# Kernel tuning notes

Hardware: AMD Instinct MI355X
Metric: run time of the kernel (lower is better)

The kernel has to match this reference:

```python
import jax, jax.numpy as jnp
import numpy as np

B, N, E = 2, 2048, 2048
H, G, D = 16, 4, 128          # num_heads, num_kv_groups, head_dim = E // H
HID = 4 * E                    # GeGLU hidden width
EPS = 1e-6


def setup_inputs() -> dict:
    key = jax.random.key(0)
    ks = jax.random.split(key, 8)
    g = lambda k, shape: jax.random.normal(k, shape, jnp.float32) * 0.02
    return {
        "x": jax.random.normal(ks[0], (B, N, E), jnp.float32),
        "wq": g(ks[1], (E, H * D)),
        "wk": g(ks[2], (E, G * D)),
        "wv": g(ks[3], (E, G * D)),
        "wo": g(ks[4], (H * D, E)),
        "w1": g(ks[5], (E, 2 * HID)),   # GeGLU in-proj (value | gate)
        "w2": g(ks[6], (HID, E)),       # GeGLU out-proj
        "norm1_w": jnp.ones((E,), jnp.float32),
        "norm2_w": jnp.ones((E,), jnp.float32),
    }


def _rope_cos_sin(n, d, dtype):
    inv_freq = 1.0 / (10000.0 ** (jnp.arange(0, d, 2, dtype=jnp.float32) / d))
    freqs = jnp.arange(n, dtype=jnp.float32)[:, None] * inv_freq[None, :]  # [n, d/2]
    emb = jnp.concatenate([freqs, freqs], axis=-1)                          # [n, d]
    return jnp.cos(emb).astype(dtype), jnp.sin(emb).astype(dtype)


def _rotate_half(t):
    d2 = t.shape[-1] // 2
    return jnp.concatenate([-t[..., d2:], t[..., :d2]], axis=-1)


def _apply_rope(t, cos, sin):
    # t: [b, h, n, d]; cos/sin: [n, d]
    return t * cos + _rotate_half(t) * sin


def _rmsnorm(x, w):
    var = jnp.mean(jnp.square(x), axis=-1, keepdims=True)
    return x * jax.lax.rsqrt(var + EPS) * w


def reference(x, wq, wk, wv, wo, w1, w2, norm1_w, norm2_w):
    b, n, _ = x.shape
    # q = k = v = x reshaped into heads (pre-projection, as in source)
    qkv = x.reshape(b, n, H, D).transpose(0, 2, 1, 3)  # [b, H, n, D]
    cos, sin = _rope_cos_sin(n, D, x.dtype)
    q_r = _apply_rope(qkv, cos, sin)
    k_r = _apply_rope(qkv, cos, sin)
    # flatten back to [b, n, E]
    q_flat = q_r.transpose(0, 2, 1, 3).reshape(b, n, E)
    k_flat = k_r.transpose(0, 2, 1, 3).reshape(b, n, E)
    v_flat = x  # v untouched by RoPE; flatten == x

    # Grouped-query attention with internal projections
    qh = (q_flat @ wq).reshape(b, n, H, D).transpose(0, 2, 1, 3)       # [b, H, n, D]
    kh = (k_flat @ wk).reshape(b, n, G, D)                              # [b, n, G, D]
    vh = (v_flat @ wv).reshape(b, n, G, D)
    kh = jnp.repeat(kh, H // G, axis=2).transpose(0, 2, 1, 3)           # [b, H, n, D]
    vh = jnp.repeat(vh, H // G, axis=2).transpose(0, 2, 1, 3)

    scale = 1.0 / np.sqrt(D)
    scores = jnp.einsum('bhqd,bhkd->bhqk', qh, kh) * scale
    attn = jax.nn.softmax(scores, axis=-1)                               # [b, H, n, n]
    ctx = jnp.einsum('bhqk,bhkd->bhqd', attn, vh)
    attn_out = ctx.transpose(0, 2, 1, 3).reshape(b, n, H * D) @ wo      # [b, n, E]

    x1 = _rmsnorm(x + attn_out, norm1_w)

    # GeGLU FFN
    uv = x1 @ w1
    u, gate = jnp.split(uv, 2, axis=-1)
    fc = (u * jax.nn.gelu(gate)) @ w2

    x2 = _rmsnorm(x1 + fc, norm2_w)
    return (x2, (k_flat, v_flat), attn)
```

## Files before the change

kernel.cpp:

```cpp
#include <hip/hip_runtime.h>
#include <hip/hip_bf16.h>


using f32x4  = __attribute__((ext_vector_type(4))) float;
using bf16x8 = __attribute__((ext_vector_type(8))) short;
using bf16x4 = __attribute__((ext_vector_type(4))) short;
using u16x4  = __attribute__((ext_vector_type(4))) unsigned short;

#define DEV __device__ __forceinline__

#define ASYNC16(lds, g)                                                        \
  __builtin_amdgcn_global_load_lds(                                           \
      (const __attribute__((address_space(1))) void*)(g),                      \
      (__attribute__((address_space(3))) void*)(lds), 16, 0, 0)

DEV unsigned short f2bf(float f) {
  unsigned int u = __float_as_uint(f);
  return (unsigned short)((u + 0x7fffu + ((u >> 16) & 1u)) >> 16);
}
DEV float bf2f(unsigned short h) {
  return __uint_as_float(((unsigned int)h) << 16);
}

DEV float waveRedSum(float v) {
#pragma unroll
  for (int o = 32; o; o >>= 1) v += __shfl_xor(v, o);
  return v;
}

__global__ __launch_bounds__(256) void kconvAll(
    const float* __restrict__ wq, const float* __restrict__ wk,
    const float* __restrict__ wv, const float* __restrict__ wo,
    const float* __restrict__ w1, unsigned short* __restrict__ dst) {
  __shared__ float tile[32][33];
  int bx = blockIdx.x * 32;
  int by = blockIdx.y * 32;
  const float* src; int nsrc, c0;
  if (bx < 2048)      { src = wq; nsrc = 2048;  c0 = bx; }
  else if (bx < 2560) { src = wk; nsrc = 512;   c0 = bx - 2048; }
  else if (bx < 3072) { src = wv; nsrc = 512;   c0 = bx - 2560; }
  else if (bx < 5120) { src = wo; nsrc = 2048;  c0 = bx - 3072; }
  else                { src = w1; nsrc = 16384; c0 = bx - 5120; }
  int tx = threadIdx.x & 31;
  int ty = threadIdx.x >> 5;
#pragma unroll
  for (int i = 0; i < 32; i += 8)
    tile[ty + i][tx] = src[(size_t)(by + ty + i) * nsrc + c0 + tx];
  __syncthreads();
#pragma unroll
  for (int i = 0; i < 32; i += 8)
    dst[(size_t)(bx + ty + i) * 2048 + by + tx] = f2bf(tile[tx][ty + i]);
}

__global__ __launch_bounds__(256) void kconvT(const float* __restrict__ in,
                                              unsigned short* __restrict__ out,
                                              int K, int N) {
  __shared__ float tile[32][33];
  int bx = blockIdx.x * 32;
  int by = blockIdx.y * 32;
  int tx = threadIdx.x & 31;
  int ty = threadIdx.x >> 5;
#pragma unroll
  for (int i = 0; i < 32; i += 8)
    tile[ty + i][tx] = in[(size_t)(by + ty + i) * N + bx + tx];
  __syncthreads();
#pragma unroll
  for (int i = 0; i < 32; i += 8)
    out[(size_t)(bx + ty + i) * K + by + tx] = f2bf(tile[tx][ty + i]);
}

__global__ __launch_bounds__(256) void krope(const float* __restrict__ x,
                                             float* __restrict__ kout,
                                             float* __restrict__ vout,
                                             unsigned short* __restrict__ xq,
                                             unsigned short* __restrict__ xb) {
  int idx = blockIdx.x * 256 + threadIdx.x;
  int f  = idx & 63;
  int h  = (idx >> 6) & 15;
  int bn = idx >> 10;
  int n  = bn & 2047;
  size_t base = (size_t)bn * 2048 + h * 128;
  float inv = exp2f((float)f * (-13.287712379549449f / 64.0f));
  float ang = (float)n * inv;
  float c = cosf(ang), s = sinf(ang);
  float a = x[base + f], b = x[base + f + 64];
  float k1 = a * c - b * s;
  float k2 = b * c + a * s;
  __builtin_nontemporal_store(k1, kout + base + f);
  __builtin_nontemporal_store(k2, kout + base + f + 64);
  xq[base + f]      = f2bf(k1);
  xq[base + f + 64] = f2bf(k2);
  __builtin_nontemporal_store(a, vout + base + f);
  __builtin_nontemporal_store(b, vout + base + f + 64);
  xb[base + f]      = f2bf(a);
  xb[base + f + 64] = f2bf(b);
}

__global__ __launch_bounds__(256) void krms1(const float* __restrict__ x,
                                             const float* __restrict__ ao,
                                             const float* __restrict__ w,
                                             unsigned short* __restrict__ x1b) {
  size_t row = blockIdx.x;
  const f32x4* xp = (const f32x4*)(x + row * 2048);
  const f32x4* ap = (const f32x4*)(ao + row * 2048);
  int tid = threadIdx.x;
  f32x4 t0 = xp[tid * 2] + ap[tid * 2];
  f32x4 t1 = xp[tid * 2 + 1] + ap[tid * 2 + 1];
  float ss = 0.f;
#pragma unroll
  for (int i = 0; i < 4; ++i) ss += t0[i] * t0[i] + t1[i] * t1[i];
  ss = waveRedSum(ss);
  __shared__ float red[4];
  int wid = tid >> 6, lane = tid & 63;
  if (!lane) red[wid] = ss;
  __syncthreads();
  ss = red[0] + red[1] + red[2] + red[3];
  float rr = rsqrtf(ss * (1.0f / 2048.0f) + 1e-6f);
  const f32x4* wp = (const f32x4*)w;
  f32x4 w0 = wp[tid * 2], w1 = wp[tid * 2 + 1];
  u16x4 o0, o1;
#pragma unroll
  for (int i = 0; i < 4; ++i) {
    o0[i] = f2bf(t0[i] * rr * w0[i]);
    o1[i] = f2bf(t1[i] * rr * w1[i]);
  }
  u16x4* op = (u16x4*)(x1b + row * 2048);
  op[tid * 2] = o0;
  op[tid * 2 + 1] = o1;
}

__global__ __launch_bounds__(256) void krms2(const unsigned short* __restrict__ x1b,
                                             const unsigned short* __restrict__ fc,
                                             const float* __restrict__ w,
                                             float* __restrict__ out) {
  size_t row = blockIdx.x;
  const u16x4* xp = (const u16x4*)(x1b + row * 2048);
  const u16x4* fp = (const u16x4*)(fc + row * 2048);
  int tid = threadIdx.x;
  u16x4 a0 = xp[tid * 2], a1 = xp[tid * 2 + 1];
  u16x4 b0 = fp[tid * 2], b1 = fp[tid * 2 + 1];
  f32x4 t0, t1;
#pragma unroll
  for (int i = 0; i < 4; ++i) {
    t0[i] = bf2f(a0[i]) + bf2f(b0[i]);
    t1[i] = bf2f(a1[i]) + bf2f(b1[i]);
  }
  float ss = 0.f;
#pragma unroll
  for (int i = 0; i < 4; ++i) ss += t0[i] * t0[i] + t1[i] * t1[i];
  ss = waveRedSum(ss);
  __shared__ float red[4];
  int wid = tid >> 6, lane = tid & 63;
  if (!lane) red[wid] = ss;
  __syncthreads();
  ss = red[0] + red[1] + red[2] + red[3];
  float rr = rsqrtf(ss * (1.0f / 2048.0f) + 1e-6f);
  const f32x4* wp = (const f32x4*)w;
  f32x4 w0 = wp[tid * 2], w1 = wp[tid * 2 + 1];
  f32x4* op = (f32x4*)(out + row * 2048);
  f32x4 o0 = t0 * rr * w0;
  f32x4 o1 = t1 * rr * w1;
  __builtin_nontemporal_store(o0, op + tid * 2);
  __builtin_nontemporal_store(o1, op + tid * 2 + 1);
}

__global__ __launch_bounds__(256, 2) void kvproj(
    const unsigned short* __restrict__ xq, const unsigned short* __restrict__ xb,
    const unsigned short* __restrict__ wkT, const unsigned short* __restrict__ wvT,
    unsigned short* __restrict__ kh, unsigned short* __restrict__ vhT) {
  const bool isV = blockIdx.z != 0;
  const unsigned short* A  = isV ? xb : xq;
  const unsigned short* Bt = isV ? wvT : wkT;
  __shared__ unsigned short As[128 * 32];
  __shared__ unsigned short Bs[128 * 32];
  const int tid = threadIdx.x;
  const int bm0 = blockIdx.y * 128, bn0 = blockIdx.x * 128;

  f32x4 acc[4][4] = {};

  const int lane = tid & 63, wid = tid >> 6;
  const int wr = wid >> 1, wc = wid & 1;
  const int lr = lane & 15, kq = lane >> 4;
  const int srow = tid >> 2;
  const int scol = (tid & 3) * 8;
  unsigned short* AsW = As + tid * 8;
  unsigned short* BsW = Bs + tid * 8;

  for (int kt = 0; kt < 2048; kt += 32) {
    ASYNC16(AsW,        A + (size_t)(bm0 + srow)      * 2048 + kt + scol);
    ASYNC16(AsW + 2048, A + (size_t)(bm0 + srow + 64) * 2048 + kt + scol);
    ASYNC16(BsW,        Bt + (size_t)(bn0 + srow)      * 2048 + kt + scol);
    ASYNC16(BsW + 2048, Bt + (size_t)(bn0 + srow + 64) * 2048 + kt + scol);
    __syncthreads();
    bf16x8 afr[4], bfr[4];
#pragma unroll
    for (int i = 0; i < 4; ++i)
      afr[i] = *(const bf16x8*)&As[(wr * 64 + i * 16 + lr) * 32 + kq * 8];
#pragma unroll
    for (int j = 0; j < 4; ++j)
      bfr[j] = *(const bf16x8*)&Bs[(wc * 64 + j * 16 + lr) * 32 + kq * 8];
#pragma unroll
    for (int i = 0; i < 4; ++i)
#pragma unroll
      for (int j = 0; j < 4; ++j)
        acc[i][j] = __builtin_amdgcn_mfma_f32_16x16x32_bf16(afr[i], bfr[j],
                                                            acc[i][j], 0, 0, 0);
    __syncthreads();
  }

#pragma unroll
  for (int i = 0; i < 4; ++i)
#pragma unroll
    for (int j = 0; j < 4; ++j) {
      int rowb = bm0 + wr * 64 + i * 16 + kq * 4;
      int col = bn0 + wc * 64 + j * 16 + lr;
#pragma unroll
      for (int r = 0; r < 4; ++r) {
        unsigned short v = f2bf(acc[i][j][r]);
        if (isV) vhT[(size_t)col * 4096 + (rowb + r)] = v;
        else     kh[(size_t)(rowb + r) * 512 + col] = v;
      }
    }
}

__global__ __launch_bounds__(512, 4) void kattn(
    const unsigned short* __restrict__ qh,
    const unsigned short* __restrict__ kh,
    const unsigned short* __restrict__ vT,
    float* __restrict__ attn,
    unsigned short* __restrict__ ctx) {
  __shared__ __align__(16) char U[65536];
  __shared__ __align__(16) char Vb[16384];
  float* redm = (float*)Vb;
  float* reds = redm + 128;

  const int tid = threadIdx.x;
  const int lane = tid & 63, w = tid >> 6;
  const int lr = lane & 15, kq = lane >> 4;
  const int bid = blockIdx.x;
  const int g8 = bid & 7;
  const int j  = bid >> 3;
  const int bz = g8 >> 2;
  const int gz = g8 & 3;
  const int hz = gz * 4 + (j & 3);
  const int q0 = (j >> 2) << 4;
  const int z  = bz * 16 + hz;

  const unsigned short* Aq =
      qh + ((size_t)(bz * 2048 + q0 + lr) * 2048 + hz * 128);
  bf16x8 qfr[4];
#pragma unroll
  for (int kk = 0; kk < 4; ++kk)
    qfr[kk] = *(const bf16x8*)(Aq + kk * 32 + kq * 8);

  const unsigned short* Kb =
      kh + ((size_t)(bz * 2048) * 512 + gz * 128);
  int krow[4], kcs[4];
#pragma unroll
  for (int R = 0; R < 4; ++R) {
    int idx = R * 64 + lane;
    krow[R] = idx >> 4;
    kcs[R] = (idx & 15) ^ (krow[R] & 7);
  }
  auto stageK = [&](int buf, int t) {
#pragma unroll
    for (int R = 0; R < 4; ++R)
      ASYNC16(U + buf * 32768 + w * 4096 + (R * 64 + lane) * 16,
              Kb + (size_t)(t * 128 + w * 16 + krow[R]) * 512 + kcs[R] * 8);
  };

  f32x4 acc[16];
#pragma unroll
  for (int t = 0; t < 16; ++t) acc[t] = f32x4{0.f, 0.f, 0.f, 0.f};

  stageK(0, 0);
  stageK(1, 1);
#pragma unroll
  for (int t = 0; t < 16; ++t) {
    if (t < 15) asm volatile("s_waitcnt vmcnt(4)" ::: "memory");
    else        asm volatile("s_waitcnt vmcnt(0)" ::: "memory");
    __builtin_amdgcn_sched_barrier(0);
    const char* Kw = U + (t & 1) * 32768 + w * 4096;
    bf16x8 kfr[4];
#pragma unroll
    for (int kk = 0; kk < 4; ++kk) {
      int cch = (kk * 4 + kq) ^ (lr & 7);
      kfr[kk] = *(const bf16x8*)(Kw + lr * 256 + cch * 16);
    }
    asm volatile("s_waitcnt lgkmcnt(0)" ::: "memory");
    __builtin_amdgcn_sched_barrier(0);
    if (t + 2 < 16) stageK(t & 1, t + 2);
    __builtin_amdgcn_s_setprio(1);
#pragma unroll
    for (int kk = 0; kk < 4; ++kk)
      acc[t] = __builtin_amdgcn_mfma_f32_16x16x32_bf16(kfr[kk], qfr[kk],
                                                       acc[t], 0, 0, 0);
    __builtin_amdgcn_s_setprio(0);
  }

  const float scale = 0.08838834764831845f;
  float mx = -3.4e38f;
#pragma unroll
  for (int t = 0; t < 16; ++t) {
    acc[t] *= scale;
#pragma unroll
    for (int r = 0; r < 4; ++r) mx = fmaxf(mx, acc[t][r]);
  }
  mx = fmaxf(mx, __shfl_xor(mx, 16));
  mx = fmaxf(mx, __shfl_xor(mx, 32));
  if (kq == 0) redm[w * 16 + lr] = mx;
  __syncthreads();
  mx = redm[lr];
#pragma unroll
  for (int ww = 1; ww < 8; ++ww) mx = fmaxf(mx, redm[ww * 16 + lr]);

  float sm = 0.f;
#pragma unroll
  for (int t = 0; t < 16; ++t) {
#pragma unroll
    for (int r = 0; r < 4; ++r) {
      float e = __expf(acc[t][r] - mx);
      acc[t][r] = e;
      sm += e;
    }
  }
  sm += __shfl_xor(sm, 16);
  sm += __shfl_xor(sm, 32);
  if (kq == 0) reds[w * 16 + lr] = sm;
  __syncthreads();
  float smt = reds[lr];
#pragma unroll
  for (int ww = 1; ww < 8; ++ww) smt += reds[ww * 16 + lr];
  float inv = 1.0f / smt;

  float* arow = attn + (((size_t)z * 2048 + q0 + lr) * 2048);
#pragma unroll
  for (int t = 0; t < 16; ++t) {
    int key = t * 128 + w * 16 + kq * 4;
    f32x4 p = acc[t] * inv;
    __builtin_nontemporal_store(p, (f32x4*)(arow + key));
    bf16x4 pb;
#pragma unroll
    for (int r = 0; r < 4; ++r) pb[r] = (short)f2bf(p[r]);
    int c8 = key >> 3;
    *(bf16x4*)(U + lr * 4096 + ((c8 ^ (lr & 7)) << 4) + ((key & 7) << 1)) = pb;
  }
  __syncthreads();

  const unsigned short* Bv = vT + (size_t)gz * 524288 + bz * 2048;
  const int d0 = w * 16;
  const int vd = lane >> 2;
  const int vcs = (lane & 3) ^ (vd & 3);
  auto stageV = [&](int buf, int t) {
    ASYNC16(Vb + buf * 8192 + w * 1024 + lane * 16,
            Bv + (size_t)(d0 + vd) * 4096 + t * 32 + vcs * 8);
  };

  f32x4 cfr = {};
  stageV(0, 0);
  stageV(1, 1);
#pragma unroll
  for (int t = 0; t < 64; ++t) {
    if (t < 63) asm volatile("s_waitcnt vmcnt(1)" ::: "memory");
    else        asm volatile("s_waitcnt vmcnt(0)" ::: "memory");
    __builtin_amdgcn_sched_barrier(0);
    int c8 = t * 4 + kq;
    bf16x8 pfr = *(const bf16x8*)(U + lr * 4096 + ((c8 ^ (lr & 7)) << 4));
    const char* Vw = Vb + (t & 1) * 8192 + w * 1024;
    bf16x8 vfr = *(const bf16x8*)(Vw + lr * 64 + ((kq ^ (lr & 3)) << 4));
    asm volatile("s_waitcnt lgkmcnt(0)" ::: "memory");
    __builtin_amdgcn_sched_barrier(0);
    if (t + 2 < 64) stageV(t & 1, t + 2);
    __builtin_amdgcn_s_setprio(1);
    cfr = __builtin_amdgcn_mfma_f32_16x16x32_bf16(pfr, vfr, cfr, 0, 0, 0);
    __builtin_amdgcn_s_setprio(0);
  }
#pragma unroll
  for (int r = 0; r < 4; ++r) {
    int q = kq * 4 + r;
    ctx[((size_t)(bz * 2048 + q0 + q) * 2048) + hz * 128 + d0 + lr] =
        f2bf(cfr[r]);
  }
}

template <bool OUT_BF16>
__global__ __launch_bounds__(512, 2) void gemm128(
    const unsigned short* __restrict__ A, const unsigned short* __restrict__ Bt,
    void* __restrict__ C_, int K, int lda, int ldb, int ldc) {
  __shared__ unsigned short As[2][128 * 64];
  __shared__ unsigned short Bs[2][128 * 64];
  const int tid = threadIdx.x;
  const int bid = blockIdx.x;
  const int xcd = bid & 7, ii = bid >> 3;
  const int my = (xcd >> 1) * 8 + (ii & 7);
  const int nx = (xcd & 1) * 8 + (ii >> 3);
  const int bm0 = my * 128, bn0 = nx * 128;
  const int lane = tid & 63, wid = tid >> 6;
  const int wr = wid >> 2, wc = wid & 3;
  const int lr = lane & 15, kq = lane >> 4;

  f32x4 acc[4][2] = {};

  int sArow[2], sAcc[2];
#pragma unroll
  for (int R = 0; R < 2; ++R) {
    int c = R * 512 + tid;
    sArow[R] = c >> 3;
    sAcc[R]  = (c & 7) ^ (sArow[R] & 7);
  }

  auto stage = [&](int buf, int k0) {
#pragma unroll
    for (int R = 0; R < 2; ++R)
      ASYNC16(&As[buf][(R * 512 + tid) * 8],
              A + (size_t)(bm0 + sArow[R]) * lda + k0 + sAcc[R] * 8);
#pragma unroll
    for (int R = 0; R < 2; ++R)
      ASYNC16(&Bs[buf][(R * 512 + tid) * 8],
              Bt + (size_t)(bn0 + sArow[R]) * ldb + k0 + sAcc[R] * 8);
  };

  const int NT = K >> 6;
  stage(0, 0);
  stage(1, 64);
  int cur = 0;
  for (int t = 0; t < NT; ++t) {
    if (t + 1 < NT) asm volatile("s_waitcnt vmcnt(4)" ::: "memory");
    else            asm volatile("s_waitcnt vmcnt(0)" ::: "memory");
    __builtin_amdgcn_sched_barrier(0);
    __builtin_amdgcn_s_barrier();
    __builtin_amdgcn_sched_barrier(0);
    const unsigned short* Ac = As[cur];
    const unsigned short* Bc = Bs[cur];
    bf16x8 afr0[4], bfr0[2];
#pragma unroll
    for (int i = 0; i < 4; ++i) {
      int row = wr * 64 + i * 16 + lr;
      afr0[i] = *(const bf16x8*)&Ac[(row * 8 + (kq ^ (row & 7))) * 8];
    }
#pragma unroll
    for (int j2 = 0; j2 < 2; ++j2) {
      int brow = wc * 32 + j2 * 16 + lr;
      bfr0[j2] = *(const bf16x8*)&Bc[(brow * 8 + (kq ^ (brow & 7))) * 8];
    }
    __builtin_amdgcn_s_setprio(1);
#pragma unroll
    for (int j2 = 0; j2 < 2; ++j2)
#pragma unroll
      for (int i = 0; i < 4; ++i)
        acc[i][j2] = __builtin_amdgcn_mfma_f32_16x16x32_bf16(afr0[i], bfr0[j2],
                                                             acc[i][j2], 0, 0, 0);
    __builtin_amdgcn_s_setprio(0);
    bf16x8 afr1[4], bfr1[2];
#pragma unroll
    for (int i = 0; i < 4; ++i) {
      int row = wr * 64 + i * 16 + lr;
      afr1[i] = *(const bf16x8*)&Ac[(row * 8 + ((4 + kq) ^ (row & 7))) * 8];
    }
#pragma unroll
    for (int j2 = 0; j2 < 2; ++j2) {
      int brow = wc * 32 + j2 * 16 + lr;
      bfr1[j2] = *(const bf16x8*)&Bc[(brow * 8 + ((4 + kq) ^ (brow & 7))) * 8];
    }
    asm volatile("s_waitcnt lgkmcnt(0)" ::: "memory");
    __builtin_amdgcn_sched_barrier(0);
    __builtin_amdgcn_s_barrier();
    __builtin_amdgcn_sched_barrier(0);
    if (t + 2 < NT) stage(cur, (t + 2) << 6);
    __builtin_amdgcn_s_setprio(1);
#pragma unroll
    for (int j2 = 0; j2 < 2; ++j2)
#pragma unroll
      for (int i = 0; i < 4; ++i)
        acc[i][j2] = __builtin_amdgcn_mfma_f32_16x16x32_bf16(afr1[i], bfr1[j2],
                                                             acc[i][j2], 0, 0, 0);
    __builtin_amdgcn_s_setprio(0);
    cur ^= 1;
  }

#pragma unroll
  for (int i = 0; i < 4; ++i)
#pragma unroll
    for (int j = 0; j < 2; ++j) {
      int rowb = bm0 + wr * 64 + i * 16 + kq * 4;
      int col = bn0 + wc * 32 + j * 16 + lr;
#pragma unroll
      for (int r = 0; r < 4; ++r) {
        if constexpr (OUT_BF16)
          ((unsigned short*)C_)[(size_t)(rowb + r) * ldc + col] = f2bf(acc[i][j][r]);
        else
          ((float*)C_)[(size_t)(rowb + r) * ldc + col] = acc[i][j][r];
      }
    }
}

__global__ __launch_bounds__(512, 2) void gemm_geglu256(
    const unsigned short* __restrict__ A, const unsigned short* __restrict__ B1,
    const unsigned short* __restrict__ B2, unsigned short* __restrict__ H_,
    int K, int lda, int ldb, int ldc) {
  __shared__ unsigned short As[2][256 * 64];
  __shared__ unsigned short B1s[2][128 * 64];
  __shared__ unsigned short B2s[2][128 * 64];
  const int tid = threadIdx.x;
  const int bid = blockIdx.x;
  const int xcd = bid & 7, ii = bid >> 3;
  const int my = (xcd >> 2) * 8 + (ii & 7);
  const int nx = (xcd & 3) * 16 + (ii >> 3);
  const int bm0 = my * 256, bn0 = nx * 128;
  const int lane = tid & 63, wid = tid >> 6;
  const int wr = wid >> 2, wc = wid & 3;
  const int lr = lane & 15, kq = lane >> 4;

  f32x4 accu[8][2] = {};
  f32x4 accg[8][2] = {};

  int sArow[4], sAcc[4], sBrow[2], sBcc[2];
#pragma unroll
  for (int R = 0; R < 4; ++R) {
    int c = R * 512 + tid;
    sArow[R] = c >> 3;
    sAcc[R]  = (c & 7) ^ (sArow[R] & 7);
  }
#pragma unroll
  for (int R = 0; R < 2; ++R) {
    int c = R * 512 + tid;
    sBrow[R] = c >> 3;
    sBcc[R]  = (c & 7) ^ (sBrow[R] & 7);
  }

  auto stage = [&](int buf, int k0) {
#pragma unroll
    for (int R = 0; R < 4; ++R)
      ASYNC16(&As[buf][(R * 512 + tid) * 8],
              A + (size_t)(bm0 + sArow[R]) * lda + k0 + sAcc[R] * 8);
#pragma unroll
    for (int R = 0; R < 2; ++R)
      ASYNC16(&B1s[buf][(R * 512 + tid) * 8],
              B1 + (size_t)(bn0 + sBrow[R]) * ldb + k0 + sBcc[R] * 8);
#pragma unroll
    for (int R = 0; R < 2; ++R)
      ASYNC16(&B2s[buf][(R * 512 + tid) * 8],
              B2 + (size_t)(bn0 + sBrow[R]) * ldb + k0 + sBcc[R] * 8);
  };

  const int NT = K >> 6;
  stage(0, 0);
  stage(1, 64);
  int cur = 0;
  for (int t = 0; t < NT; ++t) {
    if (t + 1 < NT) asm volatile("s_waitcnt vmcnt(8)" ::: "memory");
    else            asm volatile("s_waitcnt vmcnt(0)" ::: "memory");
    __builtin_amdgcn_sched_barrier(0);
    __builtin_amdgcn_s_barrier();
    __builtin_amdgcn_sched_barrier(0);
    const unsigned short* Ac = As[cur];
    const unsigned short* B1c = B1s[cur];
    const unsigned short* B2c = B2s[cur];
    bf16x8 afr0[8], b10[2], b20[2];
#pragma unroll
    for (int i = 0; i < 8; ++i) {
      int row = wr * 128 + i * 16 + lr;
      afr0[i] = *(const bf16x8*)&Ac[(row * 8 + (kq ^ (row & 7))) * 8];
    }
#pragma unroll
    for (int j2 = 0; j2 < 2; ++j2) {
      int brow = wc * 32 + j2 * 16 + lr;
      b10[j2] = *(const bf16x8*)&B1c[(brow * 8 + (kq ^ (brow & 7))) * 8];
      b20[j2] = *(const bf16x8*)&B2c[(brow * 8 + (kq ^ (brow & 7))) * 8];
    }
    __builtin_amdgcn_s_setprio(1);
#pragma unroll
    for (int j2 = 0; j2 < 2; ++j2)
#pragma unroll
      for (int i = 0; i < 8; ++i) {
        accu[i][j2] = __builtin_amdgcn_mfma_f32_16x16x32_bf16(afr0[i], b10[j2],
                                                              accu[i][j2], 0, 0, 0);
        accg[i][j2] = __builtin_amdgcn_mfma_f32_16x16x32_bf16(afr0[i], b20[j2],
                                                              accg[i][j2], 0, 0, 0);
      }
    __builtin_amdgcn_s_setprio(0);
    bf16x8 afr1[8], b11[2], b21[2];
#pragma unroll
    for (int i = 0; i < 8; ++i) {
      int row = wr * 128 + i * 16 + lr;
      afr1[i] = *(const bf16x8*)&Ac[(row * 8 + ((4 + kq) ^ (row & 7))) * 8];
    }
#pragma unroll
    for (int j2 = 0; j2 < 2; ++j2) {
      int brow = wc * 32 + j2 * 16 + lr;
      b11[j2] = *(const bf16x8*)&B1c[(brow * 8 + ((4 + kq) ^ (brow & 7))) * 8];
      b21[j2] = *(const bf16x8*)&B2c[(brow * 8 + ((4 + kq) ^ (brow & 7))) * 8];
    }
    asm volatile("s_waitcnt lgkmcnt(0)" ::: "memory");
    __builtin_amdgcn_sched_barrier(0);
    __builtin_amdgcn_s_barrier();
    __builtin_amdgcn_sched_barrier(0);
    if (t + 2 < NT) stage(cur, (t + 2) << 6);
    __builtin_amdgcn_s_setprio(1);
#pragma unroll
    for (int j2 = 0; j2 < 2; ++j2)
#pragma unroll
      for (int i = 0; i < 8; ++i) {
        accu[i][j2] = __builtin_amdgcn_mfma_f32_16x16x32_bf16(afr1[i], b11[j2],
                                                              accu[i][j2], 0, 0, 0);
        accg[i][j2] = __builtin_amdgcn_mfma_f32_16x16x32_bf16(afr1[i], b21[j2],
                                                              accg[i][j2], 0, 0, 0);
      }
    __builtin_amdgcn_s_setprio(0);
    cur ^= 1;
  }

#pragma unroll
  for (int i = 0; i < 8; ++i)
#pragma unroll
    for (int j = 0; j < 2; ++j) {
      int rowb = bm0 + wr * 128 + i * 16 + kq * 4;
      int col = bn0 + wc * 32 + j * 16 + lr;
#pragma unroll
      for (int r = 0; r < 4; ++r) {
        float u = accu[i][j][r];
        float g = accg[i][j][r];
        float tv = tanhf(0.7978845608028654f * (g + 0.044715f * g * g * g));
        float hv = u * 0.5f * g * (1.0f + tv);
        H_[(size_t)(rowb + r) * ldc + col] = f2bf(hv);
      }
    }
}

extern "C" void kernel_launch(void* const* d_in, const int* in_sizes, int n_in,
                              void* d_out, int out_size, void* d_ws, size_t ws_size,
                              hipStream_t stream) {
  const float* x   = (const float*)d_in[0];
  const float* wq  = (const float*)d_in[1];
  const float* wk  = (const float*)d_in[2];
  const float* wv  = (const float*)d_in[3];
  const float* wo  = (const float*)d_in[4];
  const float* w1  = (const float*)d_in[5];
  const float* w2  = (const float*)d_in[6];
  const float* n1w = (const float*)d_in[7];
  const float* n2w = (const float*)d_in[8];

  float* out    = (float*)d_out;
  float* x2_out = out;
  float* k_out  = out + 8388608;
  float* v_out  = out + 16777216;
  float* attn   = out + 25165824;

  char* ws = (char*)d_ws;
  unsigned short* wqT  = (unsigned short*)(ws + 0);
  unsigned short* wkT  = (unsigned short*)(ws + 8388608);
  unsigned short* wvT  = (unsigned short*)(ws + 10485760);
  unsigned short* woT  = (unsigned short*)(ws + 12582912);
  unsigned short* w1T  = (unsigned short*)(ws + 20971520);
  unsigned short* w2T  = (unsigned short*)(ws + 88080384);
  unsigned short* qh   = (unsigned short*)(ws + 121634816);
  unsigned short* kh   = (unsigned short*)(ws + 138412032);
  unsigned short* vhT  = (unsigned short*)(ws + 142606336);
  unsigned short* ctx  = (unsigned short*)(ws + 146800640);
  float*          ao   = (float*)(ws + 163577856);
  unsigned short* hbuf = (unsigned short*)(ws + 121634816);
  unsigned short* x1b  = (unsigned short*)(ws + 197132288);
  unsigned short* fc   = (unsigned short*)(ws + 213909504);

  unsigned short* xb = (unsigned short*)attn;
  unsigned short* xq = xb + 8388608;

  dim3 blk(256);
  dim3 blk512(512);

  kconvAll<<<dim3(672, 64), blk, 0, stream>>>(wq, wk, wv, wo, w1, wqT);
  kconvT<<<dim3(64, 256), blk, 0, stream>>>(w2, w2T, 8192, 2048);

  krope<<<16384, blk, 0, stream>>>(x, k_out, v_out, xq, xb);

  gemm128<true><<<dim3(512), blk512, 0, stream>>>(
      xq, wqT, qh, 2048, 2048, 2048, 2048);
  kvproj<<<dim3(4, 32, 2), blk, 0, stream>>>(xq, xb, wkT, wvT, kh, vhT);

  kattn<<<dim3(4096), blk512, 0, stream>>>(qh, kh, vhT, attn, ctx);

  gemm128<false><<<dim3(512), blk512, 0, stream>>>(
      ctx, woT, (void*)ao, 2048, 2048, 2048, 2048);
  krms1<<<4096, blk, 0, stream>>>(x, ao, n1w, x1b);
  gemm_geglu256<<<dim3(1024), blk512, 0, stream>>>(
      x1b, w1T, w1T + 16777216, hbuf, 2048, 2048, 2048, 8192);
  gemm128<true><<<dim3(512), blk512, 0, stream>>>(
      hbuf, w2T, fc, 8192, 8192, 8192, 2048);
  krms2<<<4096, blk, 0, stream>>>(x1b, fc, n2w, x2_out);
}
```

Before: 913.2 us.

## Double-buffer kvproj loads, merge softmax reductions, emit bf16 attention-out projection

The K/V projection GEMM now double-buffers its LDS tiles, using a swizzled layout and explicit vmcnt waits so global-to-LDS copies overlap with MFMA work. The attention kernel merges its max and sum cross-wave reductions into one barrier by rescaling per-wave partial sums with an online-softmax correction. The Wo projection now writes bf16 instead of fp32, which halves the traffic into the RMSNorm kernel at the cost of rounding the attention output before the residual add.

```diff
diff --git a/kernel.cpp b/kernel.cpp
--- a/kernel.cpp
+++ b/kernel.cpp
@@ -97,15 +97,21 @@
 }
 
 __global__ __launch_bounds__(256) void krms1(const float* __restrict__ x,
-                                             const float* __restrict__ ao,
+                                             const unsigned short* __restrict__ ao,
                                              const float* __restrict__ w,
                                              unsigned short* __restrict__ x1b) {
   size_t row = blockIdx.x;
   const f32x4* xp = (const f32x4*)(x + row * 2048);
-  const f32x4* ap = (const f32x4*)(ao + row * 2048);
+  const u16x4* ap = (const u16x4*)(ao + row * 2048);
   int tid = threadIdx.x;
-  f32x4 t0 = xp[tid * 2] + ap[tid * 2];
-  f32x4 t1 = xp[tid * 2 + 1] + ap[tid * 2 + 1];
+  f32x4 x0 = xp[tid * 2], x1v = xp[tid * 2 + 1];
+  u16x4 a0 = ap[tid * 2], a1 = ap[tid * 2 + 1];
+  f32x4 t0, t1;
+#pragma unroll
+  for (int i = 0; i < 4; ++i) {
+    t0[i] = x0[i] + bf2f(a0[i]);
+    t1[i] = x1v[i] + bf2f(a1[i]);
+  }
   float ss = 0.f;
 #pragma unroll
   for (int i = 0; i < 4; ++i) ss += t0[i] * t0[i] + t1[i] * t1[i];
@@ -171,8 +177,8 @@
   const bool isV = blockIdx.z != 0;
   const unsigned short* A  = isV ? xb : xq;
   const unsigned short* Bt = isV ? wvT : wkT;
-  __shared__ unsigned short As[128 * 32];
-  __shared__ unsigned short Bs[128 * 32];
+  __shared__ unsigned short As[2][128 * 32];
+  __shared__ unsigned short Bs[2][128 * 32];
   const int tid = threadIdx.x;
   const int bm0 = blockIdx.y * 128, bn0 = blockIdx.x * 128;
 
@@ -181,31 +187,62 @@
   const int lane = tid & 63, wid = tid >> 6;
   const int wr = wid >> 1, wc = wid & 1;
   const int lr = lane & 15, kq = lane >> 4;
-  const int srow = tid >> 2;
-  const int scol = (tid & 3) * 8;
-  unsigned short* AsW = As + tid * 8;
-  unsigned short* BsW = Bs + tid * 8;
-
-  for (int kt = 0; kt < 2048; kt += 32) {
-    ASYNC16(AsW,        A + (size_t)(bm0 + srow)      * 2048 + kt + scol);
-    ASYNC16(AsW + 2048, A + (size_t)(bm0 + srow + 64) * 2048 + kt + scol);
-    ASYNC16(BsW,        Bt + (size_t)(bn0 + srow)      * 2048 + kt + scol);
-    ASYNC16(BsW + 2048, Bt + (size_t)(bn0 + srow + 64) * 2048 + kt + scol);
-    __syncthreads();
+
+  int srow[2], scc[2];
+#pragma unroll
+  for (int R = 0; R < 2; ++R) {
+    int slot = R * 256 + tid;
+    srow[R] = slot >> 2;
+    scc[R]  = (slot & 3) ^ (srow[R] & 3);
+  }
+  auto stage = [&](int buf, int k0) {
+#pragma unroll
+    for (int R = 0; R < 2; ++R)
+      ASYNC16(&As[buf][(R * 256 + tid) * 8],
+              A + (size_t)(bm0 + srow[R]) * 2048 + k0 + scc[R] * 8);
+#pragma unroll
+    for (int R = 0; R < 2; ++R)
+      ASYNC16(&Bs[buf][(R * 256 + tid) * 8],
+              Bt + (size_t)(bn0 + srow[R]) * 2048 + k0 + scc[R] * 8);
+  };
+
+  const int NT = 64;
+  stage(0, 0);
+  stage(1, 32);
+  int cur = 0;
+  for (int t = 0; t < NT; ++t) {
+    if (t + 1 < NT) asm volatile("s_waitcnt vmcnt(4)" ::: "memory");
+    else            asm volatile("s_waitcnt vmcnt(0)" ::: "memory");
+    __builtin_amdgcn_sched_barrier(0);
+    __builtin_amdgcn_s_barrier();
+    __builtin_amdgcn_sched_barrier(0);
+    const unsigned short* Ac = As[cur];
+    const unsigned short* Bc = Bs[cur];
     bf16x8 afr[4], bfr[4];
 #pragma unroll
-    for (int i = 0; i < 4; ++i)
-      afr[i] = *(const bf16x8*)&As[(wr * 64 + i * 16 + lr) * 32 + kq * 8];
-#pragma unroll
-    for (int j = 0; j < 4; ++j)
-      bfr[j] = *(const bf16x8*)&Bs[(wc * 64 + j * 16 + lr) * 32 + kq * 8];
+    for (int i = 0; i < 4; ++i) {
+      int row = wr * 64 + i * 16 + lr;
+      afr[i] = *(const bf16x8*)&Ac[row * 32 + ((kq ^ (row & 3)) * 8)];
+    }
+#pragma unroll
+    for (int j = 0; j < 4; ++j) {
+      int brow = wc * 64 + j * 16 + lr;
+      bfr[j] = *(const bf16x8*)&Bc[brow * 32 + ((kq ^ (brow & 3)) * 8)];
+    }
+    asm volatile("s_waitcnt lgkmcnt(0)" ::: "memory");
+    __builtin_amdgcn_sched_barrier(0);
+    __builtin_amdgcn_s_barrier();
+    __builtin_amdgcn_sched_barrier(0);
+    if (t + 2 < NT) stage(cur, (t + 2) * 32);
+    __builtin_amdgcn_s_setprio(1);
 #pragma unroll
     for (int i = 0; i < 4; ++i)
 #pragma unroll
       for (int j = 0; j < 4; ++j)
         acc[i][j] = __builtin_amdgcn_mfma_f32_16x16x32_bf16(afr[i], bfr[j],
                                                             acc[i][j], 0, 0, 0);
-    __syncthreads();
+    __builtin_amdgcn_s_setprio(0);
+    cur ^= 1;
   }
 
 #pragma unroll
@@ -308,12 +345,6 @@
   }
   mx = fmaxf(mx, __shfl_xor(mx, 16));
   mx = fmaxf(mx, __shfl_xor(mx, 32));
-  if (kq == 0) redm[w * 16 + lr] = mx;
-  __syncthreads();
-  mx = redm[lr];
-#pragma unroll
-  for (int ww = 1; ww < 8; ++ww) mx = fmaxf(mx, redm[ww * 16 + lr]);
-
   float sm = 0.f;
 #pragma unroll
   for (int t = 0; t < 16; ++t) {
@@ -326,18 +357,22 @@
   }
   sm += __shfl_xor(sm, 16);
   sm += __shfl_xor(sm, 32);
-  if (kq == 0) reds[w * 16 + lr] = sm;
+  if (kq == 0) { redm[w * 16 + lr] = mx; reds[w * 16 + lr] = sm; }
   __syncthreads();
-  float smt = reds[lr];
-#pragma unroll
-  for (int ww = 1; ww < 8; ++ww) smt += reds[ww * 16 + lr];
-  float inv = 1.0f / smt;
+  float m = redm[lr];
+#pragma unroll
+  for (int ww = 1; ww < 8; ++ww) m = fmaxf(m, redm[ww * 16 + lr]);
+  float s = 0.f;
+#pragma unroll
+  for (int ww = 0; ww < 8; ++ww)
+    s += reds[ww * 16 + lr] * __expf(redm[ww * 16 + lr] - m);
+  float invw = __expf(mx - m) / s;
 
   float* arow = attn + (((size_t)z * 2048 + q0 + lr) * 2048);
 #pragma unroll
   for (int t = 0; t < 16; ++t) {
     int key = t * 128 + w * 16 + kq * 4;
-    f32x4 p = acc[t] * inv;
+    f32x4 p = acc[t] * invw;
     __builtin_nontemporal_store(p, (f32x4*)(arow + key));
     bf16x4 pb;
 #pragma unroll
@@ -657,7 +692,7 @@
   unsigned short* kh   = (unsigned short*)(ws + 138412032);
   unsigned short* vhT  = (unsigned short*)(ws + 142606336);
   unsigned short* ctx  = (unsigned short*)(ws + 146800640);
-  float*          ao   = (float*)(ws + 163577856);
+  unsigned short* aob  = (unsigned short*)(ws + 163577856);
   unsigned short* hbuf = (unsigned short*)(ws + 121634816);
   unsigned short* x1b  = (unsigned short*)(ws + 197132288);
   unsigned short* fc   = (unsigned short*)(ws + 213909504);
@@ -679,9 +714,9 @@
 
   kattn<<<dim3(4096), blk512, 0, stream>>>(qh, kh, vhT, attn, ctx);
 
-  gemm128<false><<<dim3(512), blk512, 0, stream>>>(
-      ctx, woT, (void*)ao, 2048, 2048, 2048, 2048);
-  krms1<<<4096, blk, 0, stream>>>(x, ao, n1w, x1b);
+  gemm128<true><<<dim3(512), blk512, 0, stream>>>(
+      ctx, woT, aob, 2048, 2048, 2048, 2048);
+  krms1<<<4096, blk, 0, stream>>>(x, aob, n1w, x1b);
   gemm_geglu256<<<dim3(1024), blk512, 0, stream>>>(
       x1b, w1T, w1T + 16777216, hbuf, 2048, 2048, 2048, 8192);
   gemm128<true><<<dim3(512), blk512, 0, stream>>>(
```

New measurement: 905.0 us. Within noise of the previous version (-0.9%).
